# Performance work log

Hardware: AMD Instinct MI355X
Metric: run time of the kernel (lower is better)

The kernel has to match this reference:

```python
import jax, jax.numpy as jnp
import numpy as np

DELTA_PULL = 0.5
DELTA_PUSH = 1.5
EPS = 1e-6


def setup_inputs() -> dict:
    key = jax.random.key(0)
    k1, k2 = jax.random.split(key)
    B, C, H, W, K = 4, 16, 512, 512, 16
    embedding_maps = jax.random.normal(k1, (B, C, H, W), dtype=jnp.float32)
    instance_masks = jax.random.randint(k2, (B, K, H, W), 0, 2, dtype=jnp.int32)
    return {"embedding_maps": embedding_maps, "instance_masks": instance_masks}


def reference(embedding_maps, instance_masks):
    emb = embedding_maps                      # [B, C, H, W]
    m = (instance_masks > 0).astype(emb.dtype)  # [B, K, H, W]
    K = m.shape[1]

    # per-instance masked segment reductions over all H*W pixels
    counts = m.sum((-1, -2))                                   # [B, K]
    sums = jnp.einsum('bchw,bkhw->bkc', emb, m)                # [B, K, C]
    sq_sums = jnp.einsum('bchw,bkhw->bkc', emb * emb, m)       # [B, K, C]

    valid = counts > 0                                          # [B, K]
    safe_counts = jnp.maximum(counts, 1.0)
    means = sums / safe_counts[..., None]                       # [B, K, C] exact fg mean

    # sum over fg pixels of ||e - mean||^2 = sq_sum - 2*mean.sum + n*mean^2
    pull_k = (sq_sums - 2.0 * means * sums + counts[..., None] * means * means).sum(-1)
    pull_k = jnp.where(valid, pull_k / (counts + EPS), 0.0)     # [B, K]

    M = valid.sum(-1).astype(emb.dtype)                         # [B] num valid instances
    pull_b = pull_k.sum(-1) / jnp.maximum(M, 1.0)               # [B]

    # pairwise push between valid instance means (i < j)
    diff = means[:, :, None, :] - means[:, None, :, :]          # [B, K, K, C]
    dist = jnp.sqrt((diff * diff).sum(-1) + 1e-12)              # [B, K, K]
    iu = jnp.arange(K)
    pair = valid[:, :, None] & valid[:, None, :] & (iu[:, None] < iu[None, :])
    push_terms = jnp.where(pair, jnp.maximum(DELTA_PUSH - dist, 0.0) ** 2, 0.0)
    npairs = M * (M - 1.0) / 2.0
    push_b = jnp.where(M > 1.0, push_terms.sum((-1, -2)) / jnp.maximum(npairs, 1.0), 0.0)

    return (DELTA_PULL * pull_b + push_b).mean()
```

## Files before the change

kernel.cpp:

```cpp
#include <hip/hip_runtime.h>

#define BB 4
#define CC 16
#define KK 16
#define HWP (512 * 512)
#define TPB 1024
#define TPW 256
#define NTILES (HWP / TPB)
#define THREADS 256
#define NSLICE 16
#define WSTOT (64 + 1024 + 1024)

typedef short bf16x8 __attribute__((ext_vector_type(8)));
typedef float f32x4 __attribute__((ext_vector_type(4)));

__device__ __forceinline__ float fmaxf_(float a, float b) { return a > b ? a : b; }

__device__ __forceinline__ unsigned short f2bf(float f) {
    unsigned u = __float_as_uint(f);
    u += 0x7FFFu + ((u >> 16) & 1u);
    return (unsigned short)(u >> 16);
}

__global__ __launch_bounds__(THREADS) void disc_mfma_kernel(
    const float* __restrict__ emb, const int* __restrict__ masks,
    float* __restrict__ ws)
{
    __shared__ __align__(16) unsigned short bits[TPB];

    const int tid = threadIdx.x;
    const int lane = tid & 63;
    const int wave = tid >> 6;
    const int b = blockIdx.x / NTILES;
    const int tile = blockIdx.x % NTILES;
    const size_t tile0 = (size_t)tile * TPB;
    const int wbase = wave * TPW;
    float* slice = ws + (size_t)((blockIdx.x * 4 + wave) & (NSLICE - 1)) * WSTOT;

    const int quad = lane >> 4;
    const int r = lane & 15;

    const int* mbase = masks + (size_t)b * KK * HWP + tile0 + wbase;
    #pragma unroll
    for (int c = 0; c < 2; ++c) {
        unsigned v0 = 0, v1 = 0;
        #pragma unroll
        for (int k = 0; k < KK; ++k) {
            int2 mm = *(const int2*)(mbase + (size_t)k * HWP + c * 128 + 2 * lane);
            v0 |= (mm.x > 0 ? 1u : 0u) << k;
            v1 |= (mm.y > 0 ? 1u : 0u) << k;
        }
        ((unsigned*)bits)[(wbase + c * 128) / 2 + lane] = v0 | (v1 << 16);
    }

    union { bf16x8 v; unsigned short s[8]; } Bones;
    #pragma unroll
    for (int i = 0; i < 8; ++i) Bones.s[i] = 0x3F80;

    const float* ebase = emb + ((size_t)b * CC + r) * HWP + tile0;

    f32x4 acc_s = {0.f, 0.f, 0.f, 0.f};
    f32x4 acc_q = {0.f, 0.f, 0.f, 0.f};
    f32x4 acc_c = {0.f, 0.f, 0.f, 0.f};

    #pragma unroll
    for (int g = 0; g < TPW / 32; ++g) {
        const int p0 = wbase + g * 32;

        uint4 bw = *(const uint4*)&bits[p0 + quad * 8];
        union { bf16x8 v; unsigned u[4]; } A;
        A.u[0] = ((bw.x >> r) & 0x00010001u) * 0x3F80u;
        A.u[1] = ((bw.y >> r) & 0x00010001u) * 0x3F80u;
        A.u[2] = ((bw.z >> r) & 0x00010001u) * 0x3F80u;
        A.u[3] = ((bw.w >> r) & 0x00010001u) * 0x3F80u;

        const float4* ep = (const float4*)(ebase + p0 + quad * 8);
        float4 f0 = ep[0], f1 = ep[1];
        const float e[8] = {f0.x, f0.y, f0.z, f0.w, f1.x, f1.y, f1.z, f1.w};
        union { bf16x8 v; unsigned short s[8]; } Bf, B2;
        #pragma unroll
        for (int i = 0; i < 8; ++i) {
            Bf.s[i] = f2bf(e[i]);
            B2.s[i] = f2bf(e[i] * e[i]);
        }

        acc_s = __builtin_amdgcn_mfma_f32_16x16x32_bf16(A.v, Bf.v, acc_s, 0, 0, 0);
        acc_q = __builtin_amdgcn_mfma_f32_16x16x32_bf16(A.v, B2.v, acc_q, 0, 0, 0);
        acc_c = __builtin_amdgcn_mfma_f32_16x16x32_bf16(A.v, Bones.v, acc_c, 0, 0, 0);
    }

    #pragma unroll
    for (int reg = 0; reg < 4; ++reg) {
        const int krow = quad * 4 + reg;
        atomicAdd(&slice[64 + ((size_t)b * KK + krow) * CC + r], acc_s[reg]);
        atomicAdd(&slice[64 + 1024 + ((size_t)b * KK + krow) * CC + r], acc_q[reg]);
    }
    if (r == 0) {
        #pragma unroll
        for (int reg = 0; reg < 4; ++reg) {
            atomicAdd(&slice[b * KK + quad * 4 + reg], acc_c[reg]);
        }
    }
}

__global__ __launch_bounds__(256) void disc_finalize_kernel(
    const float* __restrict__ ws, float* __restrict__ out)
{
    __shared__ float red[WSTOT];
    __shared__ float means[BB][KK][CC];
    __shared__ float partial[BB];
    const int tid = threadIdx.x;

    for (int idx = tid; idx < WSTOT; idx += 256) {
        float t = 0.f;
        #pragma unroll
        for (int s = 0; s < NSLICE; ++s) t += ws[(size_t)s * WSTOT + idx];
        red[idx] = t;
    }
    __syncthreads();

    const float* red_cnt = red;
    const float* red_sum = red + 64;
    const float* red_sq  = red + 64 + 1024;

    const int b = tid >> 6;
    const int lane = tid & 63;

    const float DELTA_PULL = 0.5f;
    const float DELTA_PUSH = 1.5f;
    const float EPS = 1e-6f;

    float cntk = 0.f;
    bool valid = false;
    float pull_k = 0.f;
    if (lane < KK) {
        int k = lane;
        cntk = red_cnt[b * KK + k];
        valid = cntk > 0.f;
        float safe = fmaxf_(cntk, 1.f);
        float acc_sq = 0.f, acc_ss = 0.f;
        #pragma unroll
        for (int c = 0; c < CC; ++c) {
            float sv = red_sum[(b * KK + k) * CC + c];
            means[b][k][c] = sv / safe;
            acc_sq += red_sq[(b * KK + k) * CC + c];
            acc_ss += sv * sv;
        }
        if (valid) pull_k = (acc_sq - acc_ss / cntk) / (cntk + EPS);
    }

    unsigned long long bal = __ballot(lane < KK && valid);
    float M = (float)__popcll(bal);

    float ps = pull_k;
    #pragma unroll
    for (int d = 32; d >= 1; d >>= 1) ps += __shfl_xor(ps, d, 64);
    float pull_b = ps / fmaxf_(M, 1.f);

    __syncthreads();

    float push = 0.f;
    for (int t = lane; t < KK * KK; t += 64) {
        int i = t >> 4, j = t & 15;
        if (i < j && ((bal >> i) & 1ull) && ((bal >> j) & 1ull)) {
            float d2 = 1e-12f;
            #pragma unroll
            for (int c = 0; c < CC; ++c) {
                float df = means[b][i][c] - means[b][j][c];
                d2 = fmaf(df, df, d2);
            }
            float dist = sqrtf(d2);
            float h = fmaxf_(DELTA_PUSH - dist, 0.f);
            push += h * h;
        }
    }
    #pragma unroll
    for (int d = 32; d >= 1; d >>= 1) push += __shfl_xor(push, d, 64);

    if (lane == 0) {
        float npairs = M * (M - 1.f) * 0.5f;
        float push_b = (M > 1.f) ? push / fmaxf_(npairs, 1.f) : 0.f;
        partial[b] = DELTA_PULL * pull_b + push_b;
    }
    __syncthreads();
    if (tid == 0) {
        out[0] = (partial[0] + partial[1] + partial[2] + partial[3]) * 0.25f;
    }
}

extern "C" void kernel_launch(void* const* d_in, const int* in_sizes, int n_in,
                              void* d_out, int out_size, void* d_ws, size_t ws_size,
                              hipStream_t stream) {
    const float* emb = (const float*)d_in[0];
    const int* masks = (const int*)d_in[1];
    float* ws = (float*)d_ws;

    hipMemsetAsync(d_ws, 0, NSLICE * WSTOT * sizeof(float), stream);

    dim3 grid(BB * NTILES);
    disc_mfma_kernel<<<grid, THREADS, 0, stream>>>(emb, masks, ws);
    disc_finalize_kernel<<<1, 256, 0, stream>>>(ws, (float*)d_out);
}
```

Baseline: 157.2 us.

## Load mask planes directly into MFMA operands, drop LDS bit-packing, issue all loads upfront

Each lane now loads its own instance's mask row with 128-bit loads and turns it straight into bf16 A-operand values, replacing the LDS bit-packing stage and its strided int2 loads. All mask and embedding loads for the wave are issued before any MFMA, so more memory traffic is in flight at once. Tiles shrink to 512 pixels per block and the atomic slice count doubles to 32 to spread contention across more blocks. This raises register use and atomic traffic in exchange for fewer, wider loads and no shared-memory round trip.

```diff
diff --git a/kernel.cpp b/kernel.cpp
--- a/kernel.cpp
+++ b/kernel.cpp
@@ -4,11 +4,11 @@
 #define CC 16
 #define KK 16
 #define HWP (512 * 512)
-#define TPB 1024
-#define TPW 256
+#define TPB 512
+#define TPW 128
 #define NTILES (HWP / TPB)
 #define THREADS 256
-#define NSLICE 16
+#define NSLICE 32
 #define WSTOT (64 + 1024 + 1024)
 
 typedef short bf16x8 __attribute__((ext_vector_type(8)));
@@ -21,74 +21,73 @@
     u += 0x7FFFu + ((u >> 16) & 1u);
     return (unsigned short)(u >> 16);
 }
+__device__ __forceinline__ unsigned pkbf(float x, float y) {
+    return (unsigned)f2bf(x) | ((unsigned)f2bf(y) << 16);
+}
+__device__ __forceinline__ unsigned pkmask(int a, int b) {
+    unsigned ua = (a > 0) ? 1u : 0u;
+    unsigned ub = (b > 0) ? 1u : 0u;
+    return (ua | (ub << 16)) * 0x3F80u;
+}
 
 __global__ __launch_bounds__(THREADS) void disc_mfma_kernel(
     const float* __restrict__ emb, const int* __restrict__ masks,
     float* __restrict__ ws)
 {
-    __shared__ __align__(16) unsigned short bits[TPB];
-
     const int tid = threadIdx.x;
     const int lane = tid & 63;
     const int wave = tid >> 6;
     const int b = blockIdx.x / NTILES;
     const int tile = blockIdx.x % NTILES;
-    const size_t tile0 = (size_t)tile * TPB;
-    const int wbase = wave * TPW;
-    float* slice = ws + (size_t)((blockIdx.x * 4 + wave) & (NSLICE - 1)) * WSTOT;
+    const size_t base_px = (size_t)tile * TPB + wave * TPW;
 
     const int quad = lane >> 4;
     const int r = lane & 15;
 
-    const int* mbase = masks + (size_t)b * KK * HWP + tile0 + wbase;
-    #pragma unroll
-    for (int c = 0; c < 2; ++c) {
-        unsigned v0 = 0, v1 = 0;
-        #pragma unroll
-        for (int k = 0; k < KK; ++k) {
-            int2 mm = *(const int2*)(mbase + (size_t)k * HWP + c * 128 + 2 * lane);
-            v0 |= (mm.x > 0 ? 1u : 0u) << k;
-            v1 |= (mm.y > 0 ? 1u : 0u) << k;
-        }
-        ((unsigned*)bits)[(wbase + c * 128) / 2 + lane] = v0 | (v1 << 16);
+    const int*   mplane = masks + ((size_t)b * KK + r) * HWP + base_px + quad * 8;
+    const float* eplane = emb   + ((size_t)b * CC + r) * HWP + base_px + quad * 8;
+
+    int4 m0[4], m1[4]; float4 e0[4], e1[4];
+    #pragma unroll
+    for (int g = 0; g < 4; ++g) {
+        const int4* mp = (const int4*)(mplane + g * 32);
+        m0[g] = mp[0]; m1[g] = mp[1];
+        const float4* ep = (const float4*)(eplane + g * 32);
+        e0[g] = ep[0]; e1[g] = ep[1];
     }
 
     union { bf16x8 v; unsigned short s[8]; } Bones;
     #pragma unroll
     for (int i = 0; i < 8; ++i) Bones.s[i] = 0x3F80;
-
-    const float* ebase = emb + ((size_t)b * CC + r) * HWP + tile0;
 
     f32x4 acc_s = {0.f, 0.f, 0.f, 0.f};
     f32x4 acc_q = {0.f, 0.f, 0.f, 0.f};
     f32x4 acc_c = {0.f, 0.f, 0.f, 0.f};
 
     #pragma unroll
-    for (int g = 0; g < TPW / 32; ++g) {
-        const int p0 = wbase + g * 32;
-
-        uint4 bw = *(const uint4*)&bits[p0 + quad * 8];
+    for (int g = 0; g < 4; ++g) {
         union { bf16x8 v; unsigned u[4]; } A;
-        A.u[0] = ((bw.x >> r) & 0x00010001u) * 0x3F80u;
-        A.u[1] = ((bw.y >> r) & 0x00010001u) * 0x3F80u;
-        A.u[2] = ((bw.z >> r) & 0x00010001u) * 0x3F80u;
-        A.u[3] = ((bw.w >> r) & 0x00010001u) * 0x3F80u;
-
-        const float4* ep = (const float4*)(ebase + p0 + quad * 8);
-        float4 f0 = ep[0], f1 = ep[1];
-        const float e[8] = {f0.x, f0.y, f0.z, f0.w, f1.x, f1.y, f1.z, f1.w};
-        union { bf16x8 v; unsigned short s[8]; } Bf, B2;
-        #pragma unroll
-        for (int i = 0; i < 8; ++i) {
-            Bf.s[i] = f2bf(e[i]);
-            B2.s[i] = f2bf(e[i] * e[i]);
-        }
+        A.u[0] = pkmask(m0[g].x, m0[g].y);
+        A.u[1] = pkmask(m0[g].z, m0[g].w);
+        A.u[2] = pkmask(m1[g].x, m1[g].y);
+        A.u[3] = pkmask(m1[g].z, m1[g].w);
+
+        union { bf16x8 v; unsigned u[4]; } Bf, B2;
+        Bf.u[0] = pkbf(e0[g].x, e0[g].y);
+        Bf.u[1] = pkbf(e0[g].z, e0[g].w);
+        Bf.u[2] = pkbf(e1[g].x, e1[g].y);
+        Bf.u[3] = pkbf(e1[g].z, e1[g].w);
+        B2.u[0] = pkbf(e0[g].x * e0[g].x, e0[g].y * e0[g].y);
+        B2.u[1] = pkbf(e0[g].z * e0[g].z, e0[g].w * e0[g].w);
+        B2.u[2] = pkbf(e1[g].x * e1[g].x, e1[g].y * e1[g].y);
+        B2.u[3] = pkbf(e1[g].z * e1[g].z, e1[g].w * e1[g].w);
 
         acc_s = __builtin_amdgcn_mfma_f32_16x16x32_bf16(A.v, Bf.v, acc_s, 0, 0, 0);
         acc_q = __builtin_amdgcn_mfma_f32_16x16x32_bf16(A.v, B2.v, acc_q, 0, 0, 0);
         acc_c = __builtin_amdgcn_mfma_f32_16x16x32_bf16(A.v, Bones.v, acc_c, 0, 0, 0);
     }
 
+    float* slice = ws + (size_t)((blockIdx.x * 4 + wave) & (NSLICE - 1)) * WSTOT;
     #pragma unroll
     for (int reg = 0; reg < 4; ++reg) {
         const int krow = quad * 4 + reg;
```

After: 170.9 us. 1.09x slower.
